# Kernel optimization log

Hardware: AMD Instinct MI355X
Metric: run time of the kernel (lower is better)

The kernel has to match this reference:

```python
import jax, jax.numpy as jnp
import numpy as np


def setup_inputs() -> dict:
    key = jax.random.key(0)
    ks = jax.random.split(key, 6)
    B, L, F, I, A = 16, 8192, 512, 512, 256
    scale = 1.0 / np.sqrt(A)
    return {
        "z": jax.random.normal(ks[0], (B, I), dtype=jnp.float32),
        "features": jax.random.normal(ks[1], (B, F, L), dtype=jnp.float32),
        "W_feat": jax.random.normal(ks[2], (A, F), dtype=jnp.float32) * (1.0 / np.sqrt(F)),
        "W_inp": jax.random.normal(ks[3], (A, I), dtype=jnp.float32) * (1.0 / np.sqrt(I)),
        "b_inp": jax.random.normal(ks[4], (A,), dtype=jnp.float32) * 0.01,
        "v_atten": jax.random.normal(ks[5], (A,), dtype=jnp.float32) * scale,
    }


def reference(z, features, W_feat, W_inp, b_inp, v_atten):
    # features: [B, F, L] -> tf: [B, L, F]
    # proj_feat: [B, L, A]; proj_inp: [B, A]
    proj_feat = jnp.einsum("bfl,af->bla", features, W_feat)
    proj_inp = z @ W_inp.T + b_inp  # [B, A]
    att = jax.nn.relu(proj_feat + proj_inp[:, None, :])  # [B, L, A]
    scores = jnp.einsum("bla,a->bl", att, v_atten)  # [B, L]
    alpha = jax.nn.softmax(scores, axis=-1)  # [B, L]
    ctx = jnp.einsum("bfl,bl->bf", features, alpha)  # [B, F]
    return ctx, alpha
```

## Files before the change

### kernel.cpp

```cpp
#include <hip/hip_runtime.h>
#include <hip/hip_bf16.h>

#define B_ 16
#define L_ 8192
#define F_ 512
#define I_ 512
#define A_ 256
#define LT 128
#define NCH 16

typedef __attribute__((ext_vector_type(4))) float f32x4;
typedef __attribute__((ext_vector_type(8))) __bf16 bf16x8;

__device__ __forceinline__ unsigned short f2bf(float f) {
  return __builtin_bit_cast(unsigned short, (__bf16)f);
}

__global__ void k_wcvt(const float* __restrict__ W, unsigned short* __restrict__ wb) {
  int i = blockIdx.x * 256 + threadIdx.x;
  float4 v = ((const float4*)W)[i];
  ushort4 d;
  d.x = f2bf(v.x); d.y = f2bf(v.y); d.z = f2bf(v.z); d.w = f2bf(v.w);
  ((ushort4*)wb)[i] = d;
}

__global__ void k_proj(const float* __restrict__ z, const float* __restrict__ Wi,
                       const float* __restrict__ bi, float* __restrict__ proj) {
  __shared__ float zb[I_];
  const int b = blockIdx.x, t = threadIdx.x;
  zb[t] = z[b * I_ + t];
  zb[t + 256] = z[b * I_ + t + 256];
  __syncthreads();
  const float4* w4 = (const float4*)(Wi + t * I_);
  float s = bi[t];
  for (int i = 0; i < I_ / 4; ++i) {
    float4 w = w4[i];
    s += w.x * zb[4*i] + w.y * zb[4*i+1] + w.z * zb[4*i+2] + w.w * zb[4*i+3];
  }
  proj[b * A_ + t] = s;
}

__global__ __launch_bounds__(512, 2) void k_main(
    const float* __restrict__ feat,
    const unsigned short* __restrict__ wbf,
    const float* __restrict__ proj,
    const float* __restrict__ vatt,
    float* __restrict__ scores_ws,
    float* __restrict__ mz_ws,
    float* __restrict__ nf_ws)
{
  constexpr int PBUF = 131072;
  constexpr int VBUF = 132096;
  constexpr int SPART = 133120;
  constexpr int SBUF = 135168;
  constexpr int WBUF = 135680;
  constexpr int MZB  = 136192;
  constexpr int NFP  = 136208;
  __shared__ __align__(16) unsigned char smem[136208 + 16384];

  const int tid  = threadIdx.x;
  const int lane = tid & 63;
  const int wid  = tid >> 6;
  const int wm   = wid >> 1;
  const int wn   = wid & 1;
  const int bx   = blockIdx.x;
  const int b    = bx >> 6;
  const int l0   = (bx & 63) * LT;

  const float* fb = feat + (size_t)b * F_ * L_;

  float* pbufF  = (float*)(smem + PBUF);
  float* vbufF  = (float*)(smem + VBUF);
  float* spartF = (float*)(smem + SPART);
  float* sbufF  = (float*)(smem + SBUF);
  float* wbufF  = (float*)(smem + WBUF);
  float* mzF    = (float*)(smem + MZB);
  float* nfpF   = (float*)(smem + NFP);

  if (tid < A_) { pbufF[tid] = proj[b * A_ + tid]; vbufF[tid] = vatt[tid]; }

  auto load_feat = [&](int c, float2* r) {
    const float* p = fb + (size_t)(32 * c + 4 * wid) * L_ + l0 + 2 * lane;
    r[0] = *(const float2*)(p);
    r[1] = *(const float2*)(p + L_);
    r[2] = *(const float2*)(p + 2 * L_);
    r[3] = *(const float2*)(p + 3 * L_);
  };
  auto write_feat = [&](int c, const float2* r) {
    const int s = 8 * c + wid;
    #pragma unroll
    for (int h = 0; h < 2; ++h) {
      const int l = 2 * lane + h;
      ushort4 d;
      d.x = f2bf(h ? r[0].y : r[0].x);
      d.y = f2bf(h ? r[1].y : r[1].x);
      d.z = f2bf(h ? r[2].y : r[2].x);
      d.w = f2bf(h ? r[3].y : r[3].x);
      *(ushort4*)(smem + (l << 10) + ((s ^ (((l >> 1) & 31) << 1)) << 3)) = d;
    }
  };
  auto load_wf = [&](int c, bf16x8* wf) {
    const unsigned short* p = wbf + (64 * wm + (lane & 15)) * F_ + 32 * c + ((lane >> 4) << 3);
    wf[0] = *(const bf16x8*)(p);
    wf[1] = *(const bf16x8*)(p + 16 * F_);
    wf[2] = *(const bf16x8*)(p + 32 * F_);
    wf[3] = *(const bf16x8*)(p + 48 * F_);
  };

  f32x4 acc[4][4];
  #pragma unroll
  for (int i = 0; i < 4; ++i)
    #pragma unroll
    for (int j = 0; j < 4; ++j) acc[i][j] = (f32x4)0.0f;

  float2 fra[4], frb[4];
  bf16x8 wfc[4], wfn[4];

  load_feat(0, fra);
  load_feat(1, frb);
  load_wf(0, wfc);
  write_feat(0, fra);
  write_feat(1, frb);
  load_feat(2, fra);
  __syncthreads();

  for (int c = 0; c < NCH; ++c) {
    if (c + 3 < NCH) load_feat(c + 3, frb);
    if (c + 1 < NCH) load_wf(c + 1, wfn);
    const int lcol = 64 * wn + (lane & 15);
    const int og = 4 * c + (lane >> 4);
    #pragma unroll
    for (int fn = 0; fn < 4; ++fn) {
      const int l = lcol + 16 * fn;
      bf16x8 bfr = *(const bf16x8*)(smem + (l << 10) + ((og ^ ((l >> 1) & 31)) << 4));
      #pragma unroll
      for (int fm = 0; fm < 4; ++fm)
        acc[fm][fn] = __builtin_amdgcn_mfma_f32_16x16x32_bf16(wfc[fm], bfr, acc[fm][fn], 0, 0, 0);
    }
    if (c + 2 < NCH) write_feat(c + 2, fra);
    __syncthreads();
    #pragma unroll
    for (int q = 0; q < 4; ++q) { fra[q] = frb[q]; wfc[q] = wfn[q]; }
  }

  float ts[4] = {0.f, 0.f, 0.f, 0.f};
  {
    const int rb = 64 * wm + ((lane >> 4) << 2);
    #pragma unroll
    for (int fm = 0; fm < 4; ++fm)
      #pragma unroll
      for (int jj = 0; jj < 4; ++jj) {
        const int a = rb + 16 * fm + jj;
        const float pa = pbufF[a];
        const float va = vbufF[a];
        #pragma unroll
        for (int fn = 0; fn < 4; ++fn) {
          float x = acc[fm][fn][jj] + pa;
          x = fmaxf(x, 0.0f);
          ts[fn] = fmaf(x, va, ts[fn]);
        }
      }
  }
  #pragma unroll
  for (int fn = 0; fn < 4; ++fn) {
    ts[fn] += __shfl_xor(ts[fn], 16);
    ts[fn] += __shfl_xor(ts[fn], 32);
  }
  if (lane < 16) {
    #pragma unroll
    for (int fn = 0; fn < 4; ++fn)
      spartF[wm * 128 + 64 * wn + 16 * fn + lane] = ts[fn];
  }
  __syncthreads();
  if (tid < 128) {
    float s = spartF[tid] + spartF[128 + tid] + spartF[256 + tid] + spartF[384 + tid];
    scores_ws[b * L_ + l0 + tid] = s;
    sbufF[tid] = s;
  }
  __syncthreads();
  if (tid < 64) {
    float m = fmaxf(sbufF[tid], sbufF[tid + 64]);
    #pragma unroll
    for (int d = 32; d > 0; d >>= 1) m = fmaxf(m, __shfl_xor(m, d));
    if (tid == 0) mzF[0] = m;
  }
  __syncthreads();
  const float Mb = mzF[0];
  if (tid < 128) wbufF[tid] = expf(sbufF[tid] - Mb);
  __syncthreads();
  if (tid < 64) {
    float zz = wbufF[tid] + wbufF[tid + 64];
    #pragma unroll
    for (int d = 32; d > 0; d >>= 1) zz += __shfl_xor(zz, d);
    if (tid == 0) mzF[1] = zz;
  }
  {
    const int fo = tid & 63;
    const int sl = tid >> 6;
    float na[8];
    #pragma unroll
    for (int e = 0; e < 8; ++e) na[e] = 0.f;
    for (int li = 0; li < 16; ++li) {
      const int l = sl * 16 + li;
      const float w = wbufF[l];
      bf16x8 fv = *(const bf16x8*)(smem + (l << 10) + ((fo ^ ((l >> 1) & 31)) << 4));
      #pragma unroll
      for (int e = 0; e < 8; ++e) na[e] = fmaf((float)fv[e], w, na[e]);
    }
    #pragma unroll
    for (int e = 0; e < 8; ++e) nfpF[sl * 512 + fo * 8 + e] = na[e];
  }
  __syncthreads();
  {
    float v = 0.f;
    #pragma unroll
    for (int s2 = 0; s2 < 8; ++s2) v += nfpF[s2 * 512 + tid];
    nf_ws[(size_t)bx * 512 + tid] = v;
  }
  if (tid == 0) { mz_ws[bx * 2] = Mb; mz_ws[bx * 2 + 1] = mzF[1]; }
}

__global__ void k_final(const float* __restrict__ scores_ws,
                        const float* __restrict__ mz_ws,
                        const float* __restrict__ nf_ws,
                        float* __restrict__ out) {
  __shared__ float scl[64];
  __shared__ float MZ[2];
  const int b = blockIdx.x, t = threadIdx.x;
  if (t < 64) {
    float m = mz_ws[(b * 64 + t) * 2];
    float z = mz_ws[(b * 64 + t) * 2 + 1];
    float M = m;
    #pragma unroll
    for (int d = 32; d > 0; d >>= 1) M = fmaxf(M, __shfl_xor(M, d));
    float sc = expf(m - M);
    float zz = z * sc;
    #pragma unroll
    for (int d = 32; d > 0; d >>= 1) zz += __shfl_xor(zz, d);
    scl[t] = sc;
    if (t == 0) { MZ[0] = M; MZ[1] = zz; }
  }
  __syncthreads();
  const float M = MZ[0];
  const float invZ = 1.0f / MZ[1];
  for (int f = t; f < F_; f += 256) {
    float a = 0.f;
    for (int i = 0; i < 64; ++i)
      a = fmaf(nf_ws[((size_t)b * 64 + i) * 512 + f], scl[i], a);
    out[b * F_ + f] = a * invZ;
  }
  const float* sr = scores_ws + (size_t)b * L_;
  float* ao = out + B_ * F_ + (size_t)b * L_;
  for (int l = t; l < L_; l += 256) {
    ao[l] = expf(sr[l] - M) * invZ;
  }
}

extern "C" void kernel_launch(void* const* d_in, const int* in_sizes, int n_in,
                              void* d_out, int out_size, void* d_ws, size_t ws_size,
                              hipStream_t stream) {
  const float* z    = (const float*)d_in[0];
  const float* feat = (const float*)d_in[1];
  const float* Wf   = (const float*)d_in[2];
  const float* Wi   = (const float*)d_in[3];
  const float* bi   = (const float*)d_in[4];
  const float* va   = (const float*)d_in[5];
  float* out = (float*)d_out;
  char* ws = (char*)d_ws;

  float* proj    = (float*)(ws + 0);
  float* scores  = (float*)(ws + 16384);
  float* mz      = (float*)(ws + 540672);
  float* nf      = (float*)(ws + 548864);
  unsigned short* wbf = (unsigned short*)(ws + 2646016);

  k_wcvt<<<128, 256, 0, stream>>>(Wf, wbf);
  k_proj<<<16, 256, 0, stream>>>(z, Wi, bi, proj);
  k_main<<<1024, 512, 0, stream>>>(feat, wbf, proj, va, scores, mz, nf);
  k_final<<<16, 256, 0, stream>>>(scores, mz, nf, out);
}
```

Baseline: 438.6 us.

## Halve main-kernel L tile to 64 and split final reduction across more blocks

Shrinks the per-block sequence tile from 128 to 64, which halves shared memory (about 69KB) and the accumulator registers. This doubles the block count to 2048 and raises the launch-bounds occupancy target to 4 blocks per CU, to hide more memory latency. It also merges the per-block softmax steps, reusing the feature buffer for partial sums, and spreads the final kernel over 128 blocks instead of 16. The trade-offs are narrower 4-byte global feature loads instead of 8-byte ones, twice as many partial results to reduce, and more loads of the weight fragments overall.

New measurement: 453.0 us. 3.3% more time.

```diff
diff --git a/kernel.cpp b/kernel.cpp
--- a/kernel.cpp
+++ b/kernel.cpp
@@ -6,8 +6,10 @@
 #define F_ 512
 #define I_ 512
 #define A_ 256
-#define LT 128
+#define LT 64
 #define NCH 16
+#define NTILE 128
+#define NBLK (B_ * NTILE)
 
 typedef __attribute__((ext_vector_type(4))) float f32x4;
 typedef __attribute__((ext_vector_type(8))) __bf16 bf16x8;
@@ -40,7 +42,7 @@
   proj[b * A_ + t] = s;
 }
 
-__global__ __launch_bounds__(512, 2) void k_main(
+__global__ __launch_bounds__(512, 4) void k_main(
     const float* __restrict__ feat,
     const unsigned short* __restrict__ wbf,
     const float* __restrict__ proj,
@@ -49,14 +51,12 @@
     float* __restrict__ mz_ws,
     float* __restrict__ nf_ws)
 {
-  constexpr int PBUF = 131072;
-  constexpr int VBUF = 132096;
-  constexpr int SPART = 133120;
-  constexpr int SBUF = 135168;
-  constexpr int WBUF = 135680;
-  constexpr int MZB  = 136192;
-  constexpr int NFP  = 136208;
-  __shared__ __align__(16) unsigned char smem[136208 + 16384];
+  constexpr int PBUF = 65536;
+  constexpr int VBUF = 66560;
+  constexpr int SPART = 67584;
+  constexpr int SBUF = 68608;
+  constexpr int MZB  = 68864;
+  __shared__ __align__(16) unsigned char smem[68880];
 
   const int tid  = threadIdx.x;
   const int lane = tid & 63;
@@ -64,8 +64,8 @@
   const int wm   = wid >> 1;
   const int wn   = wid & 1;
   const int bx   = blockIdx.x;
-  const int b    = bx >> 6;
-  const int l0   = (bx & 63) * LT;
+  const int b    = bx >> 7;
+  const int l0   = (bx & 127) * LT;
 
   const float* fb = feat + (size_t)b * F_ * L_;
 
@@ -73,31 +73,24 @@
   float* vbufF  = (float*)(smem + VBUF);
   float* spartF = (float*)(smem + SPART);
   float* sbufF  = (float*)(smem + SBUF);
-  float* wbufF  = (float*)(smem + WBUF);
   float* mzF    = (float*)(smem + MZB);
-  float* nfpF   = (float*)(smem + NFP);
+  float* nfpF   = (float*)(smem + 0);
 
   if (tid < A_) { pbufF[tid] = proj[b * A_ + tid]; vbufF[tid] = vatt[tid]; }
 
-  auto load_feat = [&](int c, float2* r) {
-    const float* p = fb + (size_t)(32 * c + 4 * wid) * L_ + l0 + 2 * lane;
-    r[0] = *(const float2*)(p);
-    r[1] = *(const float2*)(p + L_);
-    r[2] = *(const float2*)(p + 2 * L_);
-    r[3] = *(const float2*)(p + 3 * L_);
+  auto load_feat = [&](int c, float* r) {
+    const float* p = fb + (size_t)(32 * c + 4 * wid) * L_ + l0 + lane;
+    r[0] = p[0];
+    r[1] = p[L_];
+    r[2] = p[2 * L_];
+    r[3] = p[3 * L_];
   };
-  auto write_feat = [&](int c, const float2* r) {
+  auto write_feat = [&](int c, const float* r) {
     const int s = 8 * c + wid;
-    #pragma unroll
-    for (int h = 0; h < 2; ++h) {
-      const int l = 2 * lane + h;
-      ushort4 d;
-      d.x = f2bf(h ? r[0].y : r[0].x);
-      d.y = f2bf(h ? r[1].y : r[1].x);
-      d.z = f2bf(h ? r[2].y : r[2].x);
-      d.w = f2bf(h ? r[3].y : r[3].x);
-      *(ushort4*)(smem + (l << 10) + ((s ^ (((l >> 1) & 31) << 1)) << 3)) = d;
-    }
+    const int l = lane;
+    ushort4 d;
+    d.x = f2bf(r[0]); d.y = f2bf(r[1]); d.z = f2bf(r[2]); d.w = f2bf(r[3]);
+    *(ushort4*)(smem + (l << 10) + ((s ^ (((l >> 1) & 31) << 1)) << 3)) = d;
   };
   auto load_wf = [&](int c, bf16x8* wf) {
     const unsigned short* p = wbf + (64 * wm + (lane & 15)) * F_ + 32 * c + ((lane >> 4) << 3);
@@ -107,13 +100,13 @@
     wf[3] = *(const bf16x8*)(p + 48 * F_);
   };
 
-  f32x4 acc[4][4];
+  f32x4 acc[4][2];
   #pragma unroll
   for (int i = 0; i < 4; ++i)
     #pragma unroll
-    for (int j = 0; j < 4; ++j) acc[i][j] = (f32x4)0.0f;
-
-  float2 fra[4], frb[4];
+    for (int j = 0; j < 2; ++j) acc[i][j] = (f32x4)0.0f;
+
+  float fra[4], frb[4];
   bf16x8 wfc[4], wfn[4];
 
   load_feat(0, fra);
@@ -127,10 +120,10 @@
   for (int c = 0; c < NCH; ++c) {
     if (c + 3 < NCH) load_feat(c + 3, frb);
     if (c + 1 < NCH) load_wf(c + 1, wfn);
-    const int lcol = 64 * wn + (lane & 15);
+    const int lcol = 32 * wn + (lane & 15);
     const int og = 4 * c + (lane >> 4);
     #pragma unroll
-    for (int fn = 0; fn < 4; ++fn) {
+    for (int fn = 0; fn < 2; ++fn) {
       const int l = lcol + 16 * fn;
       bf16x8 bfr = *(const bf16x8*)(smem + (l << 10) + ((og ^ ((l >> 1) & 31)) << 4));
       #pragma unroll
@@ -143,7 +136,7 @@
     for (int q = 0; q < 4; ++q) { fra[q] = frb[q]; wfc[q] = wfn[q]; }
   }
 
-  float ts[4] = {0.f, 0.f, 0.f, 0.f};
+  float ts[2] = {0.f, 0.f};
   {
     const int rb = 64 * wm + ((lane >> 4) << 2);
     #pragma unroll
@@ -154,7 +147,7 @@
         const float pa = pbufF[a];
         const float va = vbufF[a];
         #pragma unroll
-        for (int fn = 0; fn < 4; ++fn) {
+        for (int fn = 0; fn < 2; ++fn) {
           float x = acc[fm][fn][jj] + pa;
           x = fmaxf(x, 0.0f);
           ts[fn] = fmaf(x, va, ts[fn]);
@@ -162,51 +155,57 @@
       }
   }
   #pragma unroll
-  for (int fn = 0; fn < 4; ++fn) {
+  for (int fn = 0; fn < 2; ++fn) {
     ts[fn] += __shfl_xor(ts[fn], 16);
     ts[fn] += __shfl_xor(ts[fn], 32);
   }
   if (lane < 16) {
     #pragma unroll
-    for (int fn = 0; fn < 4; ++fn)
-      spartF[wm * 128 + 64 * wn + 16 * fn + lane] = ts[fn];
-  }
-  __syncthreads();
-  if (tid < 128) {
-    float s = spartF[tid] + spartF[128 + tid] + spartF[256 + tid] + spartF[384 + tid];
+    for (int fn = 0; fn < 2; ++fn)
+      spartF[wm * 64 + 32 * wn + 16 * fn + lane] = ts[fn];
+  }
+  __syncthreads();
+  if (tid < 64) {
+    float s = spartF[tid] + spartF[64 + tid] + spartF[128 + tid] + spartF[192 + tid];
     scores_ws[b * L_ + l0 + tid] = s;
     sbufF[tid] = s;
   }
   __syncthreads();
+  float wexp = 0.f;
   if (tid < 64) {
-    float m = fmaxf(sbufF[tid], sbufF[tid + 64]);
+    const float s = sbufF[tid];
+    float m = s;
     #pragma unroll
     for (int d = 32; d > 0; d >>= 1) m = fmaxf(m, __shfl_xor(m, d));
-    if (tid == 0) mzF[0] = m;
-  }
-  __syncthreads();
-  const float Mb = mzF[0];
-  if (tid < 128) wbufF[tid] = expf(sbufF[tid] - Mb);
-  __syncthreads();
-  if (tid < 64) {
-    float zz = wbufF[tid] + wbufF[tid + 64];
+    wexp = expf(s - m);
+    sbufF[tid] = wexp;
+    float zz = wexp;
     #pragma unroll
     for (int d = 32; d > 0; d >>= 1) zz += __shfl_xor(zz, d);
-    if (tid == 0) mzF[1] = zz;
-  }
+    if (tid == 0) { mzF[0] = m; mzF[1] = zz; }
+  }
+  __syncthreads();
+  float na[8];
   {
     const int fo = tid & 63;
     const int sl = tid >> 6;
-    float na[8];
     #pragma unroll
     for (int e = 0; e < 8; ++e) na[e] = 0.f;
-    for (int li = 0; li < 16; ++li) {
-      const int l = sl * 16 + li;
-      const float w = wbufF[l];
+    #pragma unroll
+    for (int li = 0; li < 8; ++li) {
+      const int l = sl * 8 + li;
+      const float w = sbufF[l];
       bf16x8 fv = *(const bf16x8*)(smem + (l << 10) + ((fo ^ ((l >> 1) & 31)) << 4));
       #pragma unroll
       for (int e = 0; e < 8; ++e) na[e] = fmaf((float)fv[e], w, na[e]);
     }
+  }
+  const float Mb = mzF[0];
+  const float Zb = mzF[1];
+  __syncthreads();
+  {
+    const int fo = tid & 63;
+    const int sl = tid >> 6;
     #pragma unroll
     for (int e = 0; e < 8; ++e) nfpF[sl * 512 + fo * 8 + e] = na[e];
   }
@@ -217,41 +216,48 @@
     for (int s2 = 0; s2 < 8; ++s2) v += nfpF[s2 * 512 + tid];
     nf_ws[(size_t)bx * 512 + tid] = v;
   }
-  if (tid == 0) { mz_ws[bx * 2] = Mb; mz_ws[bx * 2 + 1] = mzF[1]; }
+  if (tid == 0) { mz_ws[bx * 2] = Mb; mz_ws[bx * 2 + 1] = Zb; }
 }
 
 __global__ void k_final(const float* __restrict__ scores_ws,
                         const float* __restrict__ mz_ws,
                         const float* __restrict__ nf_ws,
                         float* __restrict__ out) {
-  __shared__ float scl[64];
-  __shared__ float MZ[2];
-  const int b = blockIdx.x, t = threadIdx.x;
+  __shared__ float sm[128], sz[128], scl[128], MZ[2];
+  const int bx = blockIdx.x, t = threadIdx.x;
+  const int b = bx >> 3, sub = bx & 7;
+  if (t < 128) {
+    sm[t] = mz_ws[(b * 128 + t) * 2];
+    sz[t] = mz_ws[(b * 128 + t) * 2 + 1];
+  }
+  __syncthreads();
   if (t < 64) {
-    float m = mz_ws[(b * 64 + t) * 2];
-    float z = mz_ws[(b * 64 + t) * 2 + 1];
-    float M = m;
-    #pragma unroll
-    for (int d = 32; d > 0; d >>= 1) M = fmaxf(M, __shfl_xor(M, d));
-    float sc = expf(m - M);
-    float zz = z * sc;
+    float m = fmaxf(sm[t], sm[t + 64]);
+    #pragma unroll
+    for (int d = 32; d > 0; d >>= 1) m = fmaxf(m, __shfl_xor(m, d));
+    float zz = sz[t] * expf(sm[t] - m) + sz[t + 64] * expf(sm[t + 64] - m);
     #pragma unroll
     for (int d = 32; d > 0; d >>= 1) zz += __shfl_xor(zz, d);
-    scl[t] = sc;
-    if (t == 0) { MZ[0] = M; MZ[1] = zz; }
+    if (t == 0) { MZ[0] = m; MZ[1] = zz; }
   }
   __syncthreads();
   const float M = MZ[0];
   const float invZ = 1.0f / MZ[1];
-  for (int f = t; f < F_; f += 256) {
+  if (t < 128) scl[t] = expf(sm[t] - M);
+  __syncthreads();
+  if (t < 64) {
+    const int f = sub * 64 + t;
     float a = 0.f;
-    for (int i = 0; i < 64; ++i)
-      a = fmaf(nf_ws[((size_t)b * 64 + i) * 512 + f], scl[i], a);
+    #pragma unroll 4
+    for (int i = 0; i < 128; ++i)
+      a = fmaf(nf_ws[((size_t)b * 128 + i) * 512 + f], scl[i], a);
     out[b * F_ + f] = a * invZ;
   }
   const float* sr = scores_ws + (size_t)b * L_;
   float* ao = out + B_ * F_ + (size_t)b * L_;
-  for (int l = t; l < L_; l += 256) {
+  #pragma unroll
+  for (int k = 0; k < 4; ++k) {
+    const int l = sub * 1024 + k * 256 + t;
     ao[l] = expf(sr[l] - M) * invZ;
   }
 }
@@ -269,13 +275,13 @@
   char* ws = (char*)d_ws;
 
   float* proj    = (float*)(ws + 0);
-  float* scores  = (float*)(ws + 16384);
-  float* mz      = (float*)(ws + 540672);
-  float* nf      = (float*)(ws + 548864);
-  unsigned short* wbf = (unsigned short*)(ws + 2646016);
+  unsigned short* wbf = (unsigned short*)(ws + 65536);
+  float* scores  = (float*)(ws + 393216);
+  float* mz      = (float*)(ws + 1048576);
+  float* nf      = (float*)(ws + 1114112);
 
   k_wcvt<<<128, 256, 0, stream>>>(Wf, wbf);
   k_proj<<<16, 256, 0, stream>>>(z, Wi, bi, proj);
-  k_main<<<1024, 512, 0, stream>>>(feat, wbf, proj, va, scores, mz, nf);
-  k_final<<<16, 256, 0, stream>>>(scores, mz, nf, out);
-}
+  k_main<<<NBLK, 512, 0, stream>>>(feat, wbf, proj, va, scores, mz, nf);
+  k_final<<<128, 256, 0, stream>>>(scores, mz, nf, out);
+}
```
